# Optimization experiments

Hardware: AMD Instinct MI355X
Metric: run time of the kernel (lower is better)

Reference implementation:

```python
import jax, jax.numpy as jnp
import numpy as np

NEG_SLOPE = 0.2
EPS = 1e-16


def gat_layer(x, src, dst, W, att, bias, heads, out_ch, concat, num_nodes, edge_weight):
    """WeightedGATConv forward (eval mode, dropout off).
    x: [N, Fin], src/dst: [E], W: [Fin, H*C], att: [H, 2C], bias: [H*C] or [C].
    """
    H, C = heads, out_ch
    xp = (x @ W).reshape(-1, H, C)           # [N, H, C]
    xi = xp[dst]                              # target features  [E, H, C]
    xj = xp[src]                              # source features  [E, H, C]
    # attention logits: (cat(xi, xj) * att).sum(-1)
    alpha = jnp.einsum('ehc,hc->eh', xi, att[:, :C]) + jnp.einsum('ehc,hc->eh', xj, att[:, C:])
    alpha = jnp.where(alpha >= 0, alpha, NEG_SLOPE * alpha)   # leaky_relu
    # segment softmax over incoming edges of each destination node
    amax = jax.ops.segment_max(alpha, dst, num_segments=num_nodes)  # [N, H]
    amax = jnp.where(jnp.isfinite(amax), amax, 0.0)
    ex = jnp.exp(alpha - amax[dst])                                  # [E, H]
    denom = jax.ops.segment_sum(ex, dst, num_segments=num_nodes)     # [N, H]
    a = ex / (denom[dst] + EPS)                                      # [E, H]
    msg = xj * a[..., None]                                          # [E, H, C]
    if edge_weight is not None:
        msg = msg * edge_weight[:, None, None]
    out = jax.ops.segment_sum(msg, dst, num_segments=num_nodes)      # [N, H, C]
    out = out.reshape(num_nodes, H * C) if concat else out.mean(axis=1)
    return out + bias


def setup_inputs() -> dict:
    key = jax.random.key(0)
    ks = jax.random.split(key, 10)
    N, E = 20000, 320000
    IN, HID, LAT, H = 512, 256, 128, 4
    C1 = HID // H
    glorot = lambda k, shp: jax.random.uniform(k, shp, jnp.float32, -1.0, 1.0) * jnp.sqrt(6.0 / (shp[-2] + shp[-1]))
    return {
        'x': jax.random.normal(ks[0], (N, IN), jnp.float32),
        'edge_index': jax.random.randint(ks[1], (2, E), 0, N, jnp.int32),
        'edge_weight': jax.random.uniform(ks[2], (E,), jnp.float32),
        'W1': glorot(ks[3], (IN, H * C1)),
        'att1': glorot(ks[4], (H, 2 * C1)),
        'b1': jnp.zeros((H * C1,), jnp.float32),
        'Wmu': glorot(ks[5], (HID, LAT)),
        'attmu': glorot(ks[6], (1, 2 * LAT)),
        'bmu': jnp.zeros((LAT,), jnp.float32),
        'Wlv': glorot(ks[7], (HID, LAT)),
        'attlv': glorot(ks[8], (1, 2 * LAT)),
        'blv': jnp.zeros((LAT,), jnp.float32),
    }


def reference(x, edge_index, edge_weight, W1, att1, b1, Wmu, attmu, bmu, Wlv, attlv, blv):
    N = x.shape[0]
    src, dst = edge_index[0], edge_index[1]
    H = att1.shape[0]
    C1 = att1.shape[1] // 2
    LAT = Wmu.shape[1]
    h = gat_layer(x, src, dst, W1, att1, b1, H, C1, True, N, edge_weight)
    h = jax.nn.elu(h)
    mu = gat_layer(h, src, dst, Wmu, attmu, bmu, 1, LAT, False, N, edge_weight)
    logvar = gat_layer(h, src, dst, Wlv, attlv, blv, 1, LAT, False, N, edge_weight)
    return (mu, logvar)
```

## Files before the change

### kernel.cpp

```cpp
#include <hip/hip_runtime.h>
#include <stdint.h>

#define NEG_SLOPE 0.2f
#define SEPS 1e-16f

typedef short bf16x8 __attribute__((ext_vector_type(8)));
typedef float f32x4 __attribute__((ext_vector_type(4)));

static __device__ __forceinline__ float bf2f(ushort u) {
  union { uint32_t i; float f; } v; v.i = ((uint32_t)u) << 16; return v.f;
}
static __device__ __forceinline__ ushort f2bf(float f) {
  uint32_t b = __float_as_uint(f);
  b += 0x7FFFu + ((b >> 16) & 1u);
  return (ushort)(b >> 16);
}
static __device__ __forceinline__ float blo(uint32_t u) { return __uint_as_float(u << 16); }
static __device__ __forceinline__ float bhi(uint32_t u) { return __uint_as_float(u & 0xFFFF0000u); }
static __device__ __forceinline__ float ldf(const void* p, size_t i, int mode) {
  return mode ? ((const float*)p)[i] : bf2f(((const ushort*)p)[i]);
}

__global__ void fill_out(float* __restrict__ out, int n, float v) {
  int i = blockIdx.x * 256 + threadIdx.x;
  if (i < n) out[i] = v;
}
__global__ void fill_i32(int* __restrict__ p, int n, int v) {
  int i = blockIdx.x * 256 + threadIdx.x;
  if (i < n) p[i] = v;
}

struct DetPtrs {
  const uint32_t* p[11];
  int n[11];
  const uint32_t* idx;
  int idxn;
};
__global__ void detect_all(DetPtrs dp, int* __restrict__ modes) {
  int b = blockIdx.x;
  __shared__ int sL, sH;
  if (threadIdx.x == 0) { sL = 0; sH = 0; }
  __syncthreads();
  if (b < 11) {
    const uint32_t* w = dp.p[b];
    int elems = dp.n[b];
    int nprobe = min(2048, elems / 2);
    int cL = 0, cH = 0;
    for (int i = threadIdx.x; i < nprobe; i += 256) {
      uint32_t v = w[i];
      uint32_t eL = (v >> 7) & 0xFFu;
      uint32_t eH = (v >> 23) & 0xFFu;
      if (eL >= 90u && eL <= 128u) cL++;
      if (eH >= 90u && eH <= 128u) cH++;
    }
    atomicAdd(&sL, cL); atomicAdd(&sH, cH);
    __syncthreads();
    if (threadIdx.x == 0) {
      int m;
      if (sL * 4 >= nprobe * 3) m = 0;
      else if (sH * 4 >= nprobe) m = 1;
      else m = 0;
      modes[b] = m;
    }
  } else {
    const uint32_t* w = dp.idx;
    int nprobe = min(4096, dp.idxn);
    int c = 0;
    for (int i = threadIdx.x; i < nprobe; i += 256)
      if ((i & 1) && w[i] == 0u) c++;
    atomicAdd(&sL, c);
    __syncthreads();
    if (threadIdx.x == 0) modes[11] = (sL * 4 >= (nprobe / 2) * 3) ? 1 : 0;
  }
}

__global__ void canon_idx(const void* __restrict__ ei, int* __restrict__ srcc,
                          int* __restrict__ dstc, int E, int N,
                          const int* __restrict__ m64) {
  int i = blockIdx.x * 256 + threadIdx.x;
  if (i >= E) return;
  int s, d;
  if (*m64) {
    s = (int)((const long long*)ei)[i];
    d = (int)((const long long*)ei)[E + i];
  } else {
    s = ((const int*)ei)[i];
    d = ((const int*)ei)[E + i];
  }
  srcc[i] = min(max(s, 0), N - 1);
  dstc[i] = min(max(d, 0), N - 1);
}
__global__ void canon_f32(const void* __restrict__ in, float* __restrict__ out,
                          int n, const int* __restrict__ mode) {
  int i = blockIdx.x * 256 + threadIdx.x;
  if (i >= n) return;
  float v = ldf(in, i, *mode);
  if (!isfinite(v)) v = 0.f;
  out[i] = v;
}
struct WTArgs {
  const void* w1; const void* wmu; const void* wlv;
  ushort* wt1; ushort* wall;
};
__global__ void canon_wt(WTArgs a, const int* __restrict__ modes) {
  int i = blockIdx.x * 256 + threadIdx.x;
  const int NW1 = 256 * 512;
  if (i < NW1) {
    int n = i >> 9, k = i & 511;
    float v = ldf(a.w1, (size_t)k * 256 + n, modes[2]);
    if (!isfinite(v)) v = 0.f;
    a.wt1[i] = f2bf(v);
  } else {
    int j = i - NW1;
    if (j >= 256 * 256) return;
    int n = j >> 8, k = j & 255;
    float v;
    if (n < 128) v = ldf(a.wmu, (size_t)k * 128 + n, modes[5]);
    else         v = ldf(a.wlv, (size_t)k * 128 + (n - 128), modes[8]);
    if (!isfinite(v)) v = 0.f;
    a.wall[j] = f2bf(v);
  }
}
struct SmallCan { const void* src[6]; float* dst[6]; int n[6]; int mi[6]; };
__global__ void canon_small(SmallCan a, const int* __restrict__ modes) {
  int b = blockIdx.x;
  int m = modes[a.mi[b]];
  const void* s = a.src[b];
  float* d = a.dst[b];
  for (int i = threadIdx.x; i < a.n[b]; i += 256) {
    float v = ldf(s, i, m);
    if (!isfinite(v)) v = 0.f;
    d[i] = v;
  }
}

__global__ void count_deg(const int* __restrict__ dstv, int* __restrict__ deg, int E) {
  int e = blockIdx.x * 256 + threadIdx.x;
  if (e < E) atomicAdd(&deg[dstv[e]], 1);
}
__global__ __launch_bounds__(1024) void scan_deg(const int* __restrict__ deg,
                                                 int* __restrict__ row_ptr,
                                                 int* __restrict__ row_cur, int N) {
  __shared__ int part[1024];
  int t = threadIdx.x;
  int chunk = (N + 1023) / 1024;
  int lo = t * chunk, hi = min(lo + chunk, N);
  int s = 0;
  for (int i = lo; i < hi; ++i) s += deg[i];
  part[t] = s;
  __syncthreads();
  for (int off = 1; off < 1024; off <<= 1) {
    int v = (t >= off) ? part[t - off] : 0;
    __syncthreads();
    part[t] += v;
    __syncthreads();
  }
  int base = (t == 0) ? 0 : part[t - 1];
  for (int i = lo; i < hi; ++i) {
    row_ptr[i] = base; row_cur[i] = base;
    base += deg[i];
  }
  if (t == 1023) row_ptr[N] = part[1023];
}
__global__ void scatter_edges(const int* __restrict__ dstv, const int* __restrict__ srcv,
                              const float* __restrict__ ew, int* __restrict__ row_cur,
                              int* __restrict__ csr_src, float* __restrict__ csr_w, int E) {
  int e = blockIdx.x * 256 + threadIdx.x;
  if (e < E) {
    int p = atomicAdd(&row_cur[dstv[e]], 1);
    csr_src[p] = srcv[e];
    csr_w[p] = ew[e];
  }
}

template <int KTOT>
__global__ __launch_bounds__(256) void gemm_mfma(
    const void* __restrict__ A, const ushort* __restrict__ WT,
    ushort* __restrict__ out, int M, int nTot,
    const int* __restrict__ modeA) {
  __shared__ ushort As[64][40];
  __shared__ ushort Bs[128][40];

  int t = threadIdx.x;
  int m0 = blockIdx.x * 64;
  int n0 = blockIdx.y * 128;
  int wid = t >> 6, l = t & 63;
  int wr = wid >> 1, wc = wid & 1;
  int mode = modeA ? *modeA : 1;

  int arow = t >> 2;
  int akoff = (t & 3) * 8;
  int srow = min(m0 + arow, M - 1);
  int brow = t >> 1;
  int bkoff = (t & 1) * 16;

  f32x4 acc[2][4];
#pragma unroll
  for (int i = 0; i < 2; ++i)
#pragma unroll
    for (int j = 0; j < 4; ++j) acc[i][j] = (f32x4){0.f, 0.f, 0.f, 0.f};

  int cl = l & 15;
  int ksl = (l >> 4) * 8;

  for (int k0 = 0; k0 < KTOT; k0 += 32) {
    if (mode) {
      const float* Af = (const float*)A + (size_t)srow * KTOT + k0 + akoff;
      float4 v0 = *(const float4*)Af;
      float4 v1 = *(const float4*)(Af + 4);
      uint4 pk;
      pk.x = (uint32_t)f2bf(v0.x) | ((uint32_t)f2bf(v0.y) << 16);
      pk.y = (uint32_t)f2bf(v0.z) | ((uint32_t)f2bf(v0.w) << 16);
      pk.z = (uint32_t)f2bf(v1.x) | ((uint32_t)f2bf(v1.y) << 16);
      pk.w = (uint32_t)f2bf(v1.z) | ((uint32_t)f2bf(v1.w) << 16);
      *(uint4*)&As[arow][akoff] = pk;
    } else {
      *(uint4*)&As[arow][akoff] =
          *(const uint4*)((const ushort*)A + (size_t)srow * KTOT + k0 + akoff);
    }
    {
      const ushort* wp = WT + (size_t)(n0 + brow) * KTOT + k0 + bkoff;
      *(uint4*)&Bs[brow][bkoff] = *(const uint4*)wp;
      *(uint4*)&Bs[brow][bkoff + 8] = *(const uint4*)(wp + 8);
    }
    __syncthreads();

    bf16x8 af[2], bfr[4];
#pragma unroll
    for (int i = 0; i < 2; ++i)
      af[i] = *(const bf16x8*)&As[wr * 32 + i * 16 + cl][ksl];
#pragma unroll
    for (int j = 0; j < 4; ++j)
      bfr[j] = *(const bf16x8*)&Bs[wc * 64 + j * 16 + cl][ksl];
#pragma unroll
    for (int i = 0; i < 2; ++i)
#pragma unroll
      for (int j = 0; j < 4; ++j)
        acc[i][j] = __builtin_amdgcn_mfma_f32_16x16x32_bf16(af[i], bfr[j], acc[i][j], 0, 0, 0);
    __syncthreads();
  }

  int rb = (l >> 4) * 4;
#pragma unroll
  for (int i = 0; i < 2; ++i)
#pragma unroll
    for (int j = 0; j < 4; ++j)
#pragma unroll
      for (int r = 0; r < 4; ++r) {
        int m = m0 + wr * 32 + i * 16 + rb + r;
        if (m < M)
          out[(size_t)m * nTot + n0 + wc * 64 + j * 16 + cl] = f2bf(acc[i][j][r]);
      }
}

__global__ void node_dots1(const ushort* __restrict__ xp, const float* __restrict__ att,
                           float* __restrict__ ad, float* __restrict__ as_, int N) {
  int idx = blockIdx.x * 256 + threadIdx.x;
  if (idx >= N * 8) return;
  int half = idx & 1, h = (idx >> 1) & 3, n = idx >> 3;
  const ushort* row = xp + (size_t)n * 256 + h * 64;
  const float* wv = att + h * 128 + half * 64;
  float s = 0.f;
#pragma unroll
  for (int c = 0; c < 64; c += 8) {
    uint4 v = *(const uint4*)(row + c);
    s += blo(v.x) * wv[c + 0] + bhi(v.x) * wv[c + 1]
       + blo(v.y) * wv[c + 2] + bhi(v.y) * wv[c + 3]
       + blo(v.z) * wv[c + 4] + bhi(v.z) * wv[c + 5]
       + blo(v.w) * wv[c + 6] + bhi(v.w) * wv[c + 7];
  }
  if (half == 0) ad[n * 4 + h] = s;
  else           as_[n * 4 + h] = s;
}
__global__ void node_dots2(const ushort* __restrict__ hp2,
                           const float* __restrict__ attmu, const float* __restrict__ attlv,
                           float* __restrict__ a4, int N) {
  int idx = blockIdx.x * 256 + threadIdx.x;
  if (idx >= N * 4) return;
  int w = idx & 3, n = idx >> 2;
  const float* at = (w < 2) ? attmu : attlv;
  const float* wv = at + ((w & 1) ? 128 : 0);
  const ushort* row = hp2 + (size_t)n * 256 + ((w < 2) ? 0 : 128);
  float s = 0.f;
#pragma unroll
  for (int c = 0; c < 128; c += 8) {
    uint4 v = *(const uint4*)(row + c);
    s += blo(v.x) * wv[c + 0] + bhi(v.x) * wv[c + 1]
       + blo(v.y) * wv[c + 2] + bhi(v.y) * wv[c + 3]
       + blo(v.z) * wv[c + 4] + bhi(v.z) * wv[c + 5]
       + blo(v.w) * wv[c + 6] + bhi(v.w) * wv[c + 7];
  }
  a4[idx] = s;
}

__global__ __launch_bounds__(256) void fused_agg1(
    const int* __restrict__ row_ptr, const int* __restrict__ csr_src,
    const float* __restrict__ csr_w,
    const float* __restrict__ ad, const float* __restrict__ as_,
    const ushort* __restrict__ xp, const float* __restrict__ b1,
    float* __restrict__ hout) {
  int n = blockIdx.x;
  int t = threadIdx.x;
  int g = t >> 5;
  int l = t & 31;
  int h = l >> 3;
  __shared__ float red_m[8][32];
  __shared__ float red_d[8][32];
  __shared__ float red_acc[8][256];

  int lo = row_ptr[n], hi = row_ptr[n + 1];
  float adv = ad[n * 4 + h];

  float m = -1e30f;
  for (int i = lo + g; i < hi; i += 8) {
    int s = csr_src[i];
    float a = adv + as_[s * 4 + h];
    a = a >= 0.f ? a : NEG_SLOPE * a;
    m = fmaxf(m, a);
  }
  red_m[g][l] = m;
  __syncthreads();
  m = red_m[0][l];
#pragma unroll
  for (int gg = 1; gg < 8; ++gg) m = fmaxf(m, red_m[gg][l]);

  float acc[8];
#pragma unroll
  for (int j = 0; j < 8; ++j) acc[j] = 0.f;
  float dsum = 0.f;
  for (int i = lo + g; i < hi; i += 8) {
    int s = csr_src[i];
    float a = adv + as_[s * 4 + h];
    a = a >= 0.f ? a : NEG_SLOPE * a;
    float ev = expf(a - m);
    dsum += ev;
    float cw = ev * csr_w[i];
    uint4 v = *(const uint4*)(xp + (size_t)s * 256 + l * 8);
    acc[0] += cw * blo(v.x); acc[1] += cw * bhi(v.x);
    acc[2] += cw * blo(v.y); acc[3] += cw * bhi(v.y);
    acc[4] += cw * blo(v.z); acc[5] += cw * bhi(v.z);
    acc[6] += cw * blo(v.w); acc[7] += cw * bhi(v.w);
  }
  red_d[g][l] = dsum;
#pragma unroll
  for (int j = 0; j < 8; ++j) red_acc[g][l * 8 + j] = acc[j];
  __syncthreads();

  float v = 0.f;
#pragma unroll
  for (int gg = 0; gg < 8; ++gg) v += red_acc[gg][t];
  int h2 = t >> 6;
  float den = 0.f;
#pragma unroll
  for (int gg = 0; gg < 8; ++gg) den += red_d[gg][h2 << 3];
  float inv = 1.0f / (den + SEPS);
  float val = v * inv + b1[t];
  hout[(size_t)n * 256 + t] = val > 0.f ? val : expm1f(val);
}

__global__ __launch_bounds__(256) void fused_agg2(
    const int* __restrict__ row_ptr, const int* __restrict__ csr_src,
    const float* __restrict__ csr_w, const float* __restrict__ a4,
    const ushort* __restrict__ hp2,
    const float* __restrict__ bmu, const float* __restrict__ blv,
    float* __restrict__ out, int N) {
  int n = blockIdx.x;
  int t = threadIdx.x;
  int sl = t >> 7;
  int u = t & 127;
  int g = u >> 4;
  int l = u & 15;
  __shared__ float red_m2[2][8];
  __shared__ float red_d2[2][8];
  __shared__ float red_acc2[2][8][128];

  int lo = row_ptr[n], hi = row_ptr[n + 1];
  float adv = a4[n * 4 + sl * 2];

  float m = -1e30f;
  for (int i = lo + g; i < hi; i += 8) {
    int s = csr_src[i];
    float a = adv + a4[s * 4 + sl * 2 + 1];
    a = a >= 0.f ? a : NEG_SLOPE * a;
    m = fmaxf(m, a);
  }
  if (l == 0) red_m2[sl][g] = m;
  __syncthreads();
  m = red_m2[sl][0];
#pragma unroll
  for (int gg = 1; gg < 8; ++gg) m = fmaxf(m, red_m2[sl][gg]);

  float acc[8];
#pragma unroll
  for (int j = 0; j < 8; ++j) acc[j] = 0.f;
  float dsum = 0.f;
  for (int i = lo + g; i < hi; i += 8) {
    int s = csr_src[i];
    float a = adv + a4[s * 4 + sl * 2 + 1];
    a = a >= 0.f ? a : NEG_SLOPE * a;
    float ev = expf(a - m);
    dsum += ev;
    float cw = ev * csr_w[i];
    uint4 v = *(const uint4*)(hp2 + (size_t)s * 256 + sl * 128 + l * 8);
    acc[0] += cw * blo(v.x); acc[1] += cw * bhi(v.x);
    acc[2] += cw * blo(v.y); acc[3] += cw * bhi(v.y);
    acc[4] += cw * blo(v.z); acc[5] += cw * bhi(v.z);
    acc[6] += cw * blo(v.w); acc[7] += cw * bhi(v.w);
  }
  if (l == 0) red_d2[sl][g] = dsum;
#pragma unroll
  for (int j = 0; j < 8; ++j) red_acc2[sl][g][l * 8 + j] = acc[j];
  __syncthreads();

  float v = 0.f;
#pragma unroll
  for (int gg = 0; gg < 8; ++gg) v += red_acc2[sl][gg][u];
  float den = 0.f;
#pragma unroll
  for (int gg = 0; gg < 8; ++gg) den += red_d2[sl][gg];
  float inv = 1.0f / (den + SEPS);
  out[(size_t)sl * N * 128 + (size_t)n * 128 + u] = v * inv + (sl ? blv[u] : bmu[u]);
}

extern "C" void kernel_launch(void* const* d_in, const int* in_sizes, int n_in,
                              void* d_out, int out_size, void* d_ws, size_t ws_size,
                              hipStream_t stream) {
  int OB = (out_size + 255) / 256;
  bool ok = (n_in == 12);
  int HID = 0, IN = 0, N = 0, LAT = 0, E = 0;
  if (ok) {
    HID = in_sizes[5];
    ok = ok && HID == 256;
    IN = HID ? in_sizes[3] / HID : 0;
    ok = ok && IN == 512 && in_sizes[3] == IN * HID;
    N = IN ? in_sizes[0] / IN : 0;
    ok = ok && N > 0 && in_sizes[0] == N * IN && (N % 4) == 0;
    LAT = in_sizes[8];
    ok = ok && LAT == 128;
    E = in_sizes[2];
    ok = ok && E > 0 && in_sizes[1] == 2 * E;
    ok = ok && in_sizes[4] == 2 * HID && in_sizes[6] == HID * LAT &&
         in_sizes[7] == 2 * LAT && in_sizes[9] == HID * LAT &&
         in_sizes[10] == 2 * LAT && in_sizes[11] == LAT &&
         out_size == 2 * N * LAT;
  }
  if (!ok) { fill_out<<<OB, 256, 0, stream>>>((float*)d_out, out_size, 2.0f); return; }

  char* p = (char*)d_ws;
  auto alloc = [&](size_t bytes) -> char* {
    char* r = p;
    p += (bytes + 255) & ~((size_t)255);
    return r;
  };
  ushort* xp_bf = (ushort*)alloc((size_t)N * HID * 2);
  float*  hreg  = (float*) alloc((size_t)N * HID * 4);
  ushort* WT1b  = (ushort*)alloc((size_t)HID * IN * 2);
  ushort* WallT = (ushort*)alloc((size_t)2 * LAT * HID * 2);
  float*  att1f = (float*) alloc((size_t)2 * HID * 4);
  float*  b1f   = (float*) alloc((size_t)HID * 4);
  float*  attmuf= (float*) alloc((size_t)2 * LAT * 4);
  float*  bmuf  = (float*) alloc((size_t)LAT * 4);
  float*  attlvf= (float*) alloc((size_t)2 * LAT * 4);
  float*  blvf  = (float*) alloc((size_t)LAT * 4);
  float*  ewf   = (float*) alloc((size_t)E * 4);
  float*  ad1   = (float*) alloc((size_t)N * 4 * 4);
  float*  as1   = (float*) alloc((size_t)N * 4 * 4);
  float*  a4    = (float*) alloc((size_t)N * 4 * 4);
  int*    srcc  = (int*)   alloc((size_t)E * 4);
  int*    dstc  = (int*)   alloc((size_t)E * 4);
  int*    csr_src=(int*)   alloc((size_t)E * 4);
  float*  csr_w = (float*) alloc((size_t)E * 4);
  int*    row_ptr=(int*)   alloc((size_t)(N + 1) * 4);
  int*    row_cur=(int*)   alloc((size_t)N * 4);
  int*    deg   = (int*)   alloc((size_t)N * 4);
  int*    modes = (int*)   alloc(16 * 4);

  size_t need = (size_t)(p - (char*)d_ws);
  if (need > ws_size) {
    fill_out<<<OB, 256, 0, stream>>>((float*)d_out, out_size, 3.0f);
    return;
  }

  ushort* hp2 = xp_bf;

  const int fidx[11] = {0, 2, 3, 4, 5, 6, 7, 8, 9, 10, 11};
  DetPtrs dp;
  for (int i = 0; i < 11; ++i) {
    dp.p[i] = (const uint32_t*)d_in[fidx[i]];
    dp.n[i] = in_sizes[fidx[i]];
  }
  dp.idx = (const uint32_t*)d_in[1];
  dp.idxn = 2 * E;
  detect_all<<<12, 256, 0, stream>>>(dp, modes);

  int EB1 = (E + 255) / 256;
  canon_idx<<<EB1, 256, 0, stream>>>(d_in[1], srcc, dstc, E, N, &modes[11]);
  canon_f32<<<EB1, 256, 0, stream>>>(d_in[2], ewf, E, &modes[1]);
  WTArgs wt;
  wt.w1 = d_in[3]; wt.wmu = d_in[6]; wt.wlv = d_in[9];
  wt.wt1 = WT1b; wt.wall = WallT;
  int wtot = HID * IN + 2 * LAT * HID;
  canon_wt<<<(wtot + 255) / 256, 256, 0, stream>>>(wt, modes);
  SmallCan sc;
  sc.src[0] = d_in[4];  sc.dst[0] = att1f;  sc.n[0] = 2 * HID; sc.mi[0] = 3;
  sc.src[1] = d_in[5];  sc.dst[1] = b1f;    sc.n[1] = HID;     sc.mi[1] = 4;
  sc.src[2] = d_in[7];  sc.dst[2] = attmuf; sc.n[2] = 2 * LAT; sc.mi[2] = 6;
  sc.src[3] = d_in[8];  sc.dst[3] = bmuf;   sc.n[3] = LAT;     sc.mi[3] = 7;
  sc.src[4] = d_in[10]; sc.dst[4] = attlvf; sc.n[4] = 2 * LAT; sc.mi[4] = 9;
  sc.src[5] = d_in[11]; sc.dst[5] = blvf;   sc.n[5] = LAT;     sc.mi[5] = 10;
  canon_small<<<6, 256, 0, stream>>>(sc, modes);

  fill_i32<<<(N + 255) / 256, 256, 0, stream>>>(deg, N, 0);

  count_deg<<<EB1, 256, 0, stream>>>(dstc, deg, E);
  scan_deg<<<1, 1024, 0, stream>>>(deg, row_ptr, row_cur, N);
  scatter_edges<<<EB1, 256, 0, stream>>>(dstc, srcc, ewf, row_cur, csr_src, csr_w, E);

  dim3 g1((N + 63) / 64, HID / 128);
  dim3 g2((N + 63) / 64, (2 * LAT) / 128);

  gemm_mfma<512><<<g1, 256, 0, stream>>>(d_in[0], WT1b, xp_bf, N, HID, &modes[0]);
  node_dots1<<<(N * 8 + 255) / 256, 256, 0, stream>>>(xp_bf, att1f, ad1, as1, N);
  fused_agg1<<<N, 256, 0, stream>>>(row_ptr, csr_src, csr_w, ad1, as1,
                                    xp_bf, b1f, hreg);

  gemm_mfma<256><<<g2, 256, 0, stream>>>(hreg, WallT, hp2, N, 2 * LAT, nullptr);
  node_dots2<<<(N * 4 + 255) / 256, 256, 0, stream>>>(hp2, attmuf, attlvf, a4, N);
  fused_agg2<<<N, 256, 0, stream>>>(row_ptr, csr_src, csr_w, a4,
                                    hp2, bmuf, blvf,
                                    (float*)d_out, N);
}
```

Measured before the change: 331.3 us.

## Use one wavefront per node in GAT aggregation and fuse edge canonicalization

Both aggregation kernels switch from one 256-thread block per destination node to one 64-lane wavefront per node (or per node and output half). Reductions use shuffles instead of shared memory and __syncthreads. Each chunk's attention weights and source indices are computed once per edge and broadcast by shuffle. The edge-index and edge-weight canonicalization kernels are also merged with the degree count into one kernel. The aim is less idle-thread waste and sync overhead at average degree 16, in exchange for less parallelism per high-degree node.

After: 303.8 us. 1.09x faster.

```diff
diff --git a/kernel.cpp b/kernel.cpp
--- a/kernel.cpp
+++ b/kernel.cpp
@@ -74,30 +74,30 @@
   }
 }
 
-__global__ void canon_idx(const void* __restrict__ ei, int* __restrict__ srcc,
-                          int* __restrict__ dstc, int E, int N,
-                          const int* __restrict__ m64) {
+__global__ void canon_edges(const void* __restrict__ ei, const void* __restrict__ ew,
+                            int* __restrict__ srcc, int* __restrict__ dstc,
+                            int* __restrict__ deg, float* __restrict__ ewf,
+                            int E, int N, const int* __restrict__ modes) {
   int i = blockIdx.x * 256 + threadIdx.x;
   if (i >= E) return;
   int s, d;
-  if (*m64) {
+  if (modes[11]) {
     s = (int)((const long long*)ei)[i];
     d = (int)((const long long*)ei)[E + i];
   } else {
     s = ((const int*)ei)[i];
     d = ((const int*)ei)[E + i];
   }
-  srcc[i] = min(max(s, 0), N - 1);
-  dstc[i] = min(max(d, 0), N - 1);
-}
-__global__ void canon_f32(const void* __restrict__ in, float* __restrict__ out,
-                          int n, const int* __restrict__ mode) {
-  int i = blockIdx.x * 256 + threadIdx.x;
-  if (i >= n) return;
-  float v = ldf(in, i, *mode);
+  s = min(max(s, 0), N - 1);
+  d = min(max(d, 0), N - 1);
+  srcc[i] = s;
+  dstc[i] = d;
+  atomicAdd(&deg[d], 1);
+  float v = ldf(ew, i, modes[1]);
   if (!isfinite(v)) v = 0.f;
-  out[i] = v;
-}
+  ewf[i] = v;
+}
+
 struct WTArgs {
   const void* w1; const void* wmu; const void* wlv;
   ushort* wt1; ushort* wall;
@@ -134,10 +134,6 @@
   }
 }
 
-__global__ void count_deg(const int* __restrict__ dstv, int* __restrict__ deg, int E) {
-  int e = blockIdx.x * 256 + threadIdx.x;
-  if (e < E) atomicAdd(&deg[dstv[e]], 1);
-}
 __global__ __launch_bounds__(1024) void scan_deg(const int* __restrict__ deg,
                                                  int* __restrict__ row_ptr,
                                                  int* __restrict__ row_cur, int N) {
@@ -293,133 +289,168 @@
   a4[idx] = s;
 }
 
-__global__ __launch_bounds__(256) void fused_agg1(
+__global__ __launch_bounds__(256) void fused_agg1_wave(
     const int* __restrict__ row_ptr, const int* __restrict__ csr_src,
     const float* __restrict__ csr_w,
     const float* __restrict__ ad, const float* __restrict__ as_,
     const ushort* __restrict__ xp, const float* __restrict__ b1,
-    float* __restrict__ hout) {
-  int n = blockIdx.x;
-  int t = threadIdx.x;
-  int g = t >> 5;
-  int l = t & 31;
-  int h = l >> 3;
-  __shared__ float red_m[8][32];
-  __shared__ float red_d[8][32];
-  __shared__ float red_acc[8][256];
+    float* __restrict__ hout, int N) {
+  int n = blockIdx.x * 4 + (threadIdx.x >> 6);
+  if (n >= N) return;
+  int lane = threadIdx.x & 63;
+  int h = lane & 3;
+  int es = lane >> 2;
+  int sg = lane >> 5, l = lane & 31, hl = l >> 3;
 
   int lo = row_ptr[n], hi = row_ptr[n + 1];
   float adv = ad[n * 4 + h];
 
   float m = -1e30f;
-  for (int i = lo + g; i < hi; i += 8) {
+  for (int i = lo + es; i < hi; i += 16) {
     int s = csr_src[i];
     float a = adv + as_[s * 4 + h];
     a = a >= 0.f ? a : NEG_SLOPE * a;
     m = fmaxf(m, a);
   }
-  red_m[g][l] = m;
-  __syncthreads();
-  m = red_m[0][l];
-#pragma unroll
-  for (int gg = 1; gg < 8; ++gg) m = fmaxf(m, red_m[gg][l]);
-
+  m = fmaxf(m, __shfl_xor(m, 4));
+  m = fmaxf(m, __shfl_xor(m, 8));
+  m = fmaxf(m, __shfl_xor(m, 16));
+  m = fmaxf(m, __shfl_xor(m, 32));
+
+  float dsum = 0.f;
   float acc[8];
 #pragma unroll
   for (int j = 0; j < 8; ++j) acc[j] = 0.f;
-  float dsum = 0.f;
-  for (int i = lo + g; i < hi; i += 8) {
-    int s = csr_src[i];
-    float a = adv + as_[s * 4 + h];
-    a = a >= 0.f ? a : NEG_SLOPE * a;
-    float ev = expf(a - m);
-    dsum += ev;
-    float cw = ev * csr_w[i];
-    uint4 v = *(const uint4*)(xp + (size_t)s * 256 + l * 8);
-    acc[0] += cw * blo(v.x); acc[1] += cw * bhi(v.x);
-    acc[2] += cw * blo(v.y); acc[3] += cw * bhi(v.y);
-    acc[4] += cw * blo(v.z); acc[5] += cw * bhi(v.z);
-    acc[6] += cw * blo(v.w); acc[7] += cw * bhi(v.w);
-  }
-  red_d[g][l] = dsum;
-#pragma unroll
-  for (int j = 0; j < 8; ++j) red_acc[g][l * 8 + j] = acc[j];
-  __syncthreads();
-
-  float v = 0.f;
-#pragma unroll
-  for (int gg = 0; gg < 8; ++gg) v += red_acc[gg][t];
-  int h2 = t >> 6;
-  float den = 0.f;
-#pragma unroll
-  for (int gg = 0; gg < 8; ++gg) den += red_d[gg][h2 << 3];
-  float inv = 1.0f / (den + SEPS);
-  float val = v * inv + b1[t];
-  hout[(size_t)n * 256 + t] = val > 0.f ? val : expm1f(val);
-}
-
-__global__ __launch_bounds__(256) void fused_agg2(
+
+  for (int cb = lo; cb < hi; cb += 16) {
+    int cn = min(16, hi - cb);
+    float cwreg = 0.f; int sreg = 0;
+    if (es < cn) {
+      int i = cb + es;
+      int s = csr_src[i];
+      sreg = s;
+      float a = adv + as_[s * 4 + h];
+      a = a >= 0.f ? a : NEG_SLOPE * a;
+      float ev = expf(a - m);
+      dsum += ev;
+      cwreg = ev * csr_w[i];
+    }
+    for (int el2 = 0; el2 < cn; el2 += 2) {
+      int el = el2 + sg;
+      int elc = min(el, cn - 1);
+      float cw = __shfl(cwreg, (elc << 2) | hl);
+      int s = __shfl(sreg, elc << 2);
+      if (el < cn) {
+        uint4 v = *(const uint4*)(xp + (size_t)s * 256 + l * 8);
+        acc[0] += cw * blo(v.x); acc[1] += cw * bhi(v.x);
+        acc[2] += cw * blo(v.y); acc[3] += cw * bhi(v.y);
+        acc[4] += cw * blo(v.z); acc[5] += cw * bhi(v.z);
+        acc[6] += cw * blo(v.w); acc[7] += cw * bhi(v.w);
+      }
+    }
+  }
+
+  dsum += __shfl_xor(dsum, 4);
+  dsum += __shfl_xor(dsum, 8);
+  dsum += __shfl_xor(dsum, 16);
+  dsum += __shfl_xor(dsum, 32);
+  float den = __shfl(dsum, hl);
+
+#pragma unroll
+  for (int j = 0; j < 8; ++j) acc[j] += __shfl_down(acc[j], 32);
+
+  if (sg == 0) {
+    float inv = 1.0f / (den + SEPS);
+#pragma unroll
+    for (int j = 0; j < 8; ++j) {
+      float val = acc[j] * inv + b1[l * 8 + j];
+      hout[(size_t)n * 256 + l * 8 + j] = val > 0.f ? val : expm1f(val);
+    }
+  }
+}
+
+__global__ __launch_bounds__(256) void fused_agg2_wave(
     const int* __restrict__ row_ptr, const int* __restrict__ csr_src,
     const float* __restrict__ csr_w, const float* __restrict__ a4,
     const ushort* __restrict__ hp2,
     const float* __restrict__ bmu, const float* __restrict__ blv,
     float* __restrict__ out, int N) {
-  int n = blockIdx.x;
-  int t = threadIdx.x;
-  int sl = t >> 7;
-  int u = t & 127;
-  int g = u >> 4;
-  int l = u & 15;
-  __shared__ float red_m2[2][8];
-  __shared__ float red_d2[2][8];
-  __shared__ float red_acc2[2][8][128];
+  int wid = blockIdx.x * 4 + (threadIdx.x >> 6);
+  int n = wid >> 1, sl = wid & 1;
+  if (n >= N) return;
+  int lane = threadIdx.x & 63;
+  int sg = lane >> 4, l = lane & 15;
 
   int lo = row_ptr[n], hi = row_ptr[n + 1];
   float adv = a4[n * 4 + sl * 2];
 
   float m = -1e30f;
-  for (int i = lo + g; i < hi; i += 8) {
+  for (int i = lo + lane; i < hi; i += 64) {
     int s = csr_src[i];
     float a = adv + a4[s * 4 + sl * 2 + 1];
     a = a >= 0.f ? a : NEG_SLOPE * a;
     m = fmaxf(m, a);
   }
-  if (l == 0) red_m2[sl][g] = m;
-  __syncthreads();
-  m = red_m2[sl][0];
-#pragma unroll
-  for (int gg = 1; gg < 8; ++gg) m = fmaxf(m, red_m2[sl][gg]);
-
+  m = fmaxf(m, __shfl_xor(m, 1));
+  m = fmaxf(m, __shfl_xor(m, 2));
+  m = fmaxf(m, __shfl_xor(m, 4));
+  m = fmaxf(m, __shfl_xor(m, 8));
+  m = fmaxf(m, __shfl_xor(m, 16));
+  m = fmaxf(m, __shfl_xor(m, 32));
+
+  float dsum = 0.f;
   float acc[8];
 #pragma unroll
   for (int j = 0; j < 8; ++j) acc[j] = 0.f;
-  float dsum = 0.f;
-  for (int i = lo + g; i < hi; i += 8) {
-    int s = csr_src[i];
-    float a = adv + a4[s * 4 + sl * 2 + 1];
-    a = a >= 0.f ? a : NEG_SLOPE * a;
-    float ev = expf(a - m);
-    dsum += ev;
-    float cw = ev * csr_w[i];
-    uint4 v = *(const uint4*)(hp2 + (size_t)s * 256 + sl * 128 + l * 8);
-    acc[0] += cw * blo(v.x); acc[1] += cw * bhi(v.x);
-    acc[2] += cw * blo(v.y); acc[3] += cw * bhi(v.y);
-    acc[4] += cw * blo(v.z); acc[5] += cw * bhi(v.z);
-    acc[6] += cw * blo(v.w); acc[7] += cw * bhi(v.w);
-  }
-  if (l == 0) red_d2[sl][g] = dsum;
-#pragma unroll
-  for (int j = 0; j < 8; ++j) red_acc2[sl][g][l * 8 + j] = acc[j];
-  __syncthreads();
-
-  float v = 0.f;
-#pragma unroll
-  for (int gg = 0; gg < 8; ++gg) v += red_acc2[sl][gg][u];
-  float den = 0.f;
-#pragma unroll
-  for (int gg = 0; gg < 8; ++gg) den += red_d2[sl][gg];
-  float inv = 1.0f / (den + SEPS);
-  out[(size_t)sl * N * 128 + (size_t)n * 128 + u] = v * inv + (sl ? blv[u] : bmu[u]);
+
+  for (int cb = lo; cb < hi; cb += 64) {
+    int cn = min(64, hi - cb);
+    float cwreg = 0.f; int sreg = 0;
+    if (lane < cn) {
+      int i = cb + lane;
+      int s = csr_src[i];
+      sreg = s;
+      float a = adv + a4[s * 4 + sl * 2 + 1];
+      a = a >= 0.f ? a : NEG_SLOPE * a;
+      float ev = expf(a - m);
+      dsum += ev;
+      cwreg = ev * csr_w[i];
+    }
+    for (int el2 = 0; el2 < cn; el2 += 4) {
+      int el = el2 + sg;
+      int elc = min(el, cn - 1);
+      float cw = __shfl(cwreg, elc);
+      int s = __shfl(sreg, elc);
+      if (el < cn) {
+        uint4 v = *(const uint4*)(hp2 + (size_t)s * 256 + sl * 128 + l * 8);
+        acc[0] += cw * blo(v.x); acc[1] += cw * bhi(v.x);
+        acc[2] += cw * blo(v.y); acc[3] += cw * bhi(v.y);
+        acc[4] += cw * blo(v.z); acc[5] += cw * bhi(v.z);
+        acc[6] += cw * blo(v.w); acc[7] += cw * bhi(v.w);
+      }
+    }
+  }
+
+  dsum += __shfl_xor(dsum, 1);
+  dsum += __shfl_xor(dsum, 2);
+  dsum += __shfl_xor(dsum, 4);
+  dsum += __shfl_xor(dsum, 8);
+  dsum += __shfl_xor(dsum, 16);
+  dsum += __shfl_xor(dsum, 32);
+
+#pragma unroll
+  for (int j = 0; j < 8; ++j) {
+    acc[j] += __shfl_down(acc[j], 32);
+    acc[j] += __shfl_down(acc[j], 16);
+  }
+
+  if (sg == 0) {
+    float inv = 1.0f / (dsum + SEPS);
+    const float* bb = sl ? blv : bmu;
+    float* op = out + (size_t)sl * N * 128 + (size_t)n * 128 + l * 8;
+#pragma unroll
+    for (int j = 0; j < 8; ++j) op[j] = acc[j] * inv + bb[l * 8 + j];
+  }
 }
 
 extern "C" void kernel_launch(void* const* d_in, const int* in_sizes, int n_in,
@@ -494,8 +525,9 @@
   detect_all<<<12, 256, 0, stream>>>(dp, modes);
 
   int EB1 = (E + 255) / 256;
-  canon_idx<<<EB1, 256, 0, stream>>>(d_in[1], srcc, dstc, E, N, &modes[11]);
-  canon_f32<<<EB1, 256, 0, stream>>>(d_in[2], ewf, E, &modes[1]);
+  fill_i32<<<(N + 255) / 256, 256, 0, stream>>>(deg, N, 0);
+  canon_edges<<<EB1, 256, 0, stream>>>(d_in[1], d_in[2], srcc, dstc, deg, ewf,
+                                       E, N, modes);
   WTArgs wt;
   wt.w1 = d_in[3]; wt.wmu = d_in[6]; wt.wlv = d_in[9];
   wt.wt1 = WT1b; wt.wall = WallT;
@@ -510,9 +542,6 @@
   sc.src[5] = d_in[11]; sc.dst[5] = blvf;   sc.n[5] = LAT;     sc.mi[5] = 10;
   canon_small<<<6, 256, 0, stream>>>(sc, modes);
 
-  fill_i32<<<(N + 255) / 256, 256, 0, stream>>>(deg, N, 0);
-
-  count_deg<<<EB1, 256, 0, stream>>>(dstc, deg, E);
   scan_deg<<<1, 1024, 0, stream>>>(deg, row_ptr, row_cur, N);
   scatter_edges<<<EB1, 256, 0, stream>>>(dstc, srcc, ewf, row_cur, csr_src, csr_w, E);
 
@@ -521,12 +550,12 @@
 
   gemm_mfma<512><<<g1, 256, 0, stream>>>(d_in[0], WT1b, xp_bf, N, HID, &modes[0]);
   node_dots1<<<(N * 8 + 255) / 256, 256, 0, stream>>>(xp_bf, att1f, ad1, as1, N);
-  fused_agg1<<<N, 256, 0, stream>>>(row_ptr, csr_src, csr_w, ad1, as1,
-                                    xp_bf, b1f, hreg);
+  fused_agg1_wave<<<(N + 3) / 4, 256, 0, stream>>>(row_ptr, csr_src, csr_w,
+                                                   ad1, as1, xp_bf, b1f, hreg, N);
 
   gemm_mfma<256><<<g2, 256, 0, stream>>>(hreg, WallT, hp2, N, 2 * LAT, nullptr);
   node_dots2<<<(N * 4 + 255) / 256, 256, 0, stream>>>(hp2, attmuf, attlvf, a4, N);
-  fused_agg2<<<N, 256, 0, stream>>>(row_ptr, csr_src, csr_w, a4,
-                                    hp2, bmuf, blvf,
-                                    (float*)d_out, N);
-}
+  fused_agg2_wave<<<(2 * N + 3) / 4, 256, 0, stream>>>(row_ptr, csr_src, csr_w, a4,
+                                                       hp2, bmuf, blvf,
+                                                       (float*)d_out, N);
+}
```
